# Performance work log

Measured on AMD Instinct MI355X. Metric: run time of the kernel, lower is better.

The kernel has to match this reference:

```python
import jax, jax.numpy as jnp
import numpy as np

N = 131072
IN, HID, OUT = 128, 256, 64
NUM_TASKS = 16
NUM_COPIES = 4
NUM_LAYERS = 3


def setup_inputs() -> dict:
    key = jax.random.key(0)
    ks = jax.random.split(key, 10)
    inputs = jax.random.normal(ks[0], (N, IN), dtype=jnp.float32)
    task_indices = jax.random.randint(ks[1], (N,), 0, NUM_TASKS, dtype=jnp.int32)
    copy_maps = jax.random.randint(ks[2], (NUM_LAYERS, NUM_TASKS), 0, NUM_COPIES, dtype=jnp.int32)
    # per-copy Linear weights, Kaiming-ish scale 1/sqrt(fan_in)
    W0 = jax.random.normal(ks[3], (NUM_COPIES, IN, HID), dtype=jnp.float32) / np.sqrt(IN)
    b0 = jax.random.normal(ks[4], (NUM_COPIES, HID), dtype=jnp.float32) * 0.01
    W1 = jax.random.normal(ks[5], (NUM_COPIES, HID, HID), dtype=jnp.float32) / np.sqrt(HID)
    b1 = jax.random.normal(ks[6], (NUM_COPIES, HID), dtype=jnp.float32) * 0.01
    W2 = jax.random.normal(ks[7], (NUM_COPIES, HID, OUT), dtype=jnp.float32) / np.sqrt(HID)
    b2 = jax.random.normal(ks[8], (NUM_COPIES, OUT), dtype=jnp.float32) * 0.01
    return {"inputs": inputs, "task_indices": task_indices, "copy_maps": copy_maps,
            "W0": W0, "b0": b0, "W1": W1, "b1": b1, "W2": W2, "b2": b2}


def _routed_layer(x, W, b, copy_idx, apply_tanh):
    # x: [N, d_in], W: [C, d_in, d_out], b: [C, d_out], copy_idx: [N]
    # Each token goes through exactly one copy's Linear. Equivalent to the
    # torch sort->per-copy-forward->unsort, expressed as masked accumulation
    # over the small fixed set of copies (avoids data-dependent shapes).
    y = jnp.zeros((x.shape[0], W.shape[2]), dtype=x.dtype)
    for c in range(W.shape[0]):
        mask = (copy_idx == c).astype(x.dtype)[:, None]  # [N, 1]
        y = y + mask * (x @ W[c] + b[c])
    return jnp.tanh(y) if apply_tanh else y


def reference(inputs, task_indices, copy_maps, W0, b0, W1, b1, W2, b2):
    x = inputs
    Ws = (W0, W1, W2)
    bs = (b0, b1, b2)
    for layer in range(NUM_LAYERS):
        copy_idx = copy_maps[layer][task_indices]  # [N] task->copy routing
        x = _routed_layer(x, Ws[layer], bs[layer], copy_idx,
                          apply_tanh=(layer != NUM_LAYERS - 1))
    return x
```

## Files before the change

kernel.cpp:

```cpp
#include <hip/hip_runtime.h>

#define N_TOK 131072
#define TILE 32
#define NT_MAX 4112

typedef __attribute__((ext_vector_type(8))) short s8v;
typedef __attribute__((ext_vector_type(4))) float f4v;
typedef unsigned short ushort_t;

__device__ __forceinline__ unsigned short f2bf(float x) {
    union { float f; unsigned u; } v; v.f = x;
    unsigned r = v.u + 0x7fffu + ((v.u >> 16) & 1u);
    return (unsigned short)(r >> 16);
}

__device__ __forceinline__ unsigned pk2(float a, float b) {
    union { float f; unsigned u; } x, y; x.f = a; y.f = b;
    return __byte_perm(x.u + 0x8000u, y.u + 0x8000u, 0x7632);
}

__device__ __forceinline__ float tanh_fast(float x) {
    float e = __expf(2.0f * x);
    float r = __builtin_amdgcn_rcpf(e + 1.0f);
    return __builtin_fmaf(-2.0f, r, 1.0f);
}

__global__ void prep_hist_kernel(const float* __restrict__ W0, const float* __restrict__ W1,
                                 const float* __restrict__ W2,
                                 ushort_t* __restrict__ W0p, ushort_t* __restrict__ W1p,
                                 ushort_t* __restrict__ W2p,
                                 const int* __restrict__ task, int* __restrict__ blockCounts) {
    if (blockIdx.x < 224) {
        int f = blockIdx.x * 256 + threadIdx.x;
        const float* src; ushort_t* dst; int K, N;
        if (f < 16384)      { src = W0; dst = W0p; K = 128; N = 256; }
        else if (f < 49152) { src = W1; dst = W1p; K = 256; N = 256; f -= 16384; }
        else                { src = W2; dst = W2p; K = 256; N = 64;  f -= 49152; }
        int fpc = (N >> 4) * (K >> 5) * 64;
        int c = f / fpc, r = f % fpc;
        int lane = r & 63;
        int kt = (r >> 6) % (K >> 5);
        int ftile = (r >> 6) / (K >> 5);
        int n = ftile * 16 + (lane & 15);
        int kbase = kt * 32 + (lane >> 4) * 8;
        const float* s = src + (size_t)c * K * N + (size_t)kbase * N + n;
        s8v pk;
#pragma unroll
        for (int j = 0; j < 8; j++) pk[j] = (short)f2bf(s[(size_t)j * N]);
        *reinterpret_cast<s8v*>(dst + ((size_t)(c * fpc + r) << 3)) = pk;
    } else {
        __shared__ int cnt[16];
        int t = threadIdx.x;
        int hb = blockIdx.x - 224;
        if (t < 16) cnt[t] = 0;
        __syncthreads();
        int base = hb * 2048 + t;
#pragma unroll
        for (int i = 0; i < 8; i++) atomicAdd(&cnt[task[base + i * 256]], 1);
        __syncthreads();
        if (t < 16) blockCounts[hb * 16 + t] = cnt[t];
    }
}

__global__ void sort_kernel(const int* __restrict__ task, const int* __restrict__ blockCounts,
                            int* __restrict__ tileTask, int* __restrict__ nT,
                            int* __restrict__ perm) {
    __shared__ int cntLds[1024];
    __shared__ int total[16], pref[16], rank[16];
    __shared__ int tokBase[16], tbase[17];
    int t = threadIdx.x, b = blockIdx.x;
    for (int i = t; i < 1024; i += 256) cntLds[i] = blockCounts[i];
    if (t < 16) rank[t] = 0;
    __syncthreads();
    if (t < 16) {
        int tot = 0, pf = 0;
#pragma unroll
        for (int bb = 0; bb < 64; bb++) {
            int v = cntLds[bb * 16 + t];
            tot += v;
            if (bb < b) pf += v;
        }
        total[t] = tot; pref[t] = pf;
    }
    __syncthreads();
    if (t == 0) {
        int tok = 0, tile = 0;
        for (int k = 0; k < 16; k++) {
            tokBase[k] = tok;
            tbase[k] = tile;
            int ntk = (total[k] + TILE - 1) / TILE;
            tok += ntk * TILE;
            tile += ntk;
        }
        tbase[16] = tile;
        if (b == 0) nT[0] = tile;
    }
    __syncthreads();
    if (b == 0) {
        for (int i = t; i < NT_MAX; i += 256) {
            int tk = 0;
            if (i < tbase[16]) {
#pragma unroll
                for (int k = 0; k < 16; k++) if (i >= tbase[k]) tk = k;
            }
            tileTask[i] = tk;
        }
    }
    int tk[8], my[8];
#pragma unroll
    for (int i = 0; i < 8; i++) {
        int idx = b * 2048 + i * 256 + t;
        tk[i] = task[idx];
        my[i] = atomicAdd(&rank[tk[i]], 1);
    }
#pragma unroll
    for (int i = 0; i < 8; i++) {
        int idx = b * 2048 + i * 256 + t;
        perm[tokBase[tk[i]] + pref[tk[i]] + my[i]] = idx;
    }
}

__launch_bounds__(512, 8)
__global__ void mlp_kernel(const float* __restrict__ x_in,
                           const int* __restrict__ cmap,
                           const float* __restrict__ b0,
                           const float* __restrict__ b1,
                           const float* __restrict__ b2,
                           const ushort_t* __restrict__ W0p,
                           const ushort_t* __restrict__ W1p,
                           const ushort_t* __restrict__ W2p,
                           const int* __restrict__ tileTask,
                           const int* __restrict__ nTp,
                           const int* __restrict__ perm,
                           float* __restrict__ out) {
    __shared__ __align__(16) ushort_t H1[8192];
    __shared__ __align__(16) ushort_t XH2[8192];
    __shared__ int toks[TILE];

    int b = blockIdx.x;
    if (b >= nTp[0]) return;
    int t = threadIdx.x;
    int task = tileTask[b];
    int c0 = cmap[task], c1 = cmap[16 + task], c2 = cmap[32 + task];

    int w = t >> 6;
    int lane = t & 63;
    int l15 = lane & 15, lq = lane >> 4;

    {
        int r = t >> 4, q = t & 15;
        int tok = perm[b * TILE + r];
        if (q == 0) toks[r] = tok;
        float4 v0 = make_float4(0.f, 0.f, 0.f, 0.f), v1 = v0;
        if ((unsigned)tok < (unsigned)N_TOK) {
            const float4* src = reinterpret_cast<const float4*>(x_in) + (size_t)tok * 32 + q * 2;
            v0 = src[0]; v1 = src[1];
        }
        int fragid = (r >> 4) * 4 + (q >> 2);
        int lanep = (r & 15) + 16 * (q & 3);
        uint4 pk;
        pk.x = pk2(v0.x, v0.y); pk.y = pk2(v0.z, v0.w);
        pk.z = pk2(v1.x, v1.y); pk.w = pk2(v1.z, v1.w);
        *reinterpret_cast<uint4*>(&XH2[(fragid * 64 + lanep) << 3]) = pk;
    }
    __syncthreads();

    {
        f4v acc[2][2];
#pragma unroll
        for (int mi = 0; mi < 2; mi++) {
            float4 bv = *reinterpret_cast<const float4*>(b0 + c0 * 256 + (2 * w + mi) * 16 + lq * 4);
#pragma unroll
            for (int nt = 0; nt < 2; nt++) {
                acc[mi][nt][0] = bv.x; acc[mi][nt][1] = bv.y;
                acc[mi][nt][2] = bv.z; acc[mi][nt][3] = bv.w;
            }
        }
        const ushort_t* Wc = W0p + (size_t)c0 * 32768;
#pragma unroll
        for (int kt = 0; kt < 4; kt++) {
            s8v wa[2];
#pragma unroll
            for (int mi = 0; mi < 2; mi++)
                wa[mi] = *reinterpret_cast<const s8v*>(Wc + ((((2 * w + mi) * 4 + kt) * 64 + lane) << 3));
            s8v xb[2];
#pragma unroll
            for (int nt = 0; nt < 2; nt++)
                xb[nt] = *reinterpret_cast<const s8v*>(&XH2[((nt * 4 + kt) * 64 + lane) << 3]);
#pragma unroll
            for (int mi = 0; mi < 2; mi++)
#pragma unroll
                for (int nt = 0; nt < 2; nt++)
                    acc[mi][nt] = __builtin_amdgcn_mfma_f32_16x16x32_bf16(wa[mi], xb[nt], acc[mi][nt], 0, 0, 0);
        }
#pragma unroll
        for (int mi = 0; mi < 2; mi++) {
            int ft = 2 * w + mi;
            int kt_h = ft >> 1;
            int lanep = l15 + 16 * ((ft & 1) * 2 + (lq >> 1));
            int j0 = (lq & 1) * 4;
#pragma unroll
            for (int nt = 0; nt < 2; nt++) {
                float t0 = tanh_fast(acc[mi][nt][0]);
                float t1 = tanh_fast(acc[mi][nt][1]);
                float t2 = tanh_fast(acc[mi][nt][2]);
                float t3 = tanh_fast(acc[mi][nt][3]);
                uint2 pk; pk.x = pk2(t0, t1); pk.y = pk2(t2, t3);
                *reinterpret_cast<uint2*>(&H1[(((nt * 8 + kt_h) * 64 + lanep) << 3) + j0]) = pk;
            }
        }
    }
    __syncthreads();

    {
        f4v acc[2][2];
#pragma unroll
        for (int mi = 0; mi < 2; mi++) {
            float4 bv = *reinterpret_cast<const float4*>(b1 + c1 * 256 + (2 * w + mi) * 16 + lq * 4);
#pragma unroll
            for (int nt = 0; nt < 2; nt++) {
                acc[mi][nt][0] = bv.x; acc[mi][nt][1] = bv.y;
                acc[mi][nt][2] = bv.z; acc[mi][nt][3] = bv.w;
            }
        }
        const ushort_t* Wc = W1p + (size_t)c1 * 65536;
#pragma unroll
        for (int kt = 0; kt < 8; kt++) {
            s8v wa[2];
#pragma unroll
            for (int mi = 0; mi < 2; mi++)
                wa[mi] = *reinterpret_cast<const s8v*>(Wc + ((((2 * w + mi) * 8 + kt) * 64 + lane) << 3));
            s8v xb[2];
#pragma unroll
            for (int nt = 0; nt < 2; nt++)
                xb[nt] = *reinterpret_cast<const s8v*>(&H1[((nt * 8 + kt) * 64 + lane) << 3]);
#pragma unroll
            for (int mi = 0; mi < 2; mi++)
#pragma unroll
                for (int nt = 0; nt < 2; nt++)
                    acc[mi][nt] = __builtin_amdgcn_mfma_f32_16x16x32_bf16(wa[mi], xb[nt], acc[mi][nt], 0, 0, 0);
        }
#pragma unroll
        for (int mi = 0; mi < 2; mi++) {
            int ft = 2 * w + mi;
            int kt_h = ft >> 1;
            int lanep = l15 + 16 * ((ft & 1) * 2 + (lq >> 1));
            int j0 = (lq & 1) * 4;
#pragma unroll
            for (int nt = 0; nt < 2; nt++) {
                float t0 = tanh_fast(acc[mi][nt][0]);
                float t1 = tanh_fast(acc[mi][nt][1]);
                float t2 = tanh_fast(acc[mi][nt][2]);
                float t3 = tanh_fast(acc[mi][nt][3]);
                uint2 pk; pk.x = pk2(t0, t1); pk.y = pk2(t2, t3);
                *reinterpret_cast<uint2*>(&XH2[(((nt * 8 + kt_h) * 64 + lanep) << 3) + j0]) = pk;
            }
        }
    }
    __syncthreads();

    {
        int mt = w & 3, nt = w >> 2;
        float4 bv = *reinterpret_cast<const float4*>(b2 + c2 * 64 + mt * 16 + lq * 4);
        f4v acc;
        acc[0] = bv.x; acc[1] = bv.y; acc[2] = bv.z; acc[3] = bv.w;
        const ushort_t* Wc = W2p + (size_t)c2 * 16384;
#pragma unroll
        for (int kt = 0; kt < 8; kt++) {
            s8v wa = *reinterpret_cast<const s8v*>(Wc + (((mt * 8 + kt) * 64 + lane) << 3));
            s8v xb = *reinterpret_cast<const s8v*>(&XH2[((nt * 8 + kt) * 64 + lane) << 3]);
            acc = __builtin_amdgcn_mfma_f32_16x16x32_bf16(wa, xb, acc, 0, 0, 0);
        }
        int tok = toks[nt * 16 + l15];
        if ((unsigned)tok < (unsigned)N_TOK) {
            float4 o;
            o.x = acc[0]; o.y = acc[1]; o.z = acc[2]; o.w = acc[3];
            *reinterpret_cast<float4*>(out + (size_t)tok * 64 + mt * 16 + lq * 4) = o;
        }
    }
}

extern "C" void kernel_launch(void* const* d_in, const int* in_sizes, int n_in,
                              void* d_out, int out_size, void* d_ws, size_t ws_size,
                              hipStream_t stream) {
    const float* inputs = (const float*)d_in[0];
    const int*   task   = (const int*)d_in[1];
    const int*   cmap   = (const int*)d_in[2];
    const float* W0     = (const float*)d_in[3];
    const float* b0     = (const float*)d_in[4];
    const float* W1     = (const float*)d_in[5];
    const float* b1     = (const float*)d_in[6];
    const float* W2     = (const float*)d_in[7];
    const float* b2     = (const float*)d_in[8];
    float* out = (float*)d_out;

    char* ws = (char*)d_ws;
    int* blockCounts = (int*)(ws + 0);
    int* nT          = (int*)(ws + 4096);
    int* tileTask    = (int*)(ws + 4160);
    int* perm        = (int*)(ws + 20608);
    ushort_t* W0p    = (ushort_t*)(ws + 546944);
    ushort_t* W1p    = (ushort_t*)(ws + 809088);
    ushort_t* W2p    = (ushort_t*)(ws + 1333376);

    prep_hist_kernel<<<288, 256, 0, stream>>>(W0, W1, W2, W0p, W1p, W2p, task, blockCounts);
    sort_kernel<<<64, 256, 0, stream>>>(task, blockCounts, tileTask, nT, perm);
    mlp_kernel<<<NT_MAX, 512, 0, stream>>>(inputs, cmap, b0, b1, b2,
                                           W0p, W1p, W2p, tileTask, nT, perm, out);
}
```

Before: 167.3 us.

## Double token tile to 64 per block to halve weight fetches per token

Raises the token tile from 32 to 64, so each block runs four N-fragments per wave and each weight fragment loaded from global memory feeds twice as many MFMAs. LDS buffers double, the launch-bounds occupancy hint drops from 8 to 4, and the grid is halved. Padding slots in perm are now set to -1 explicitly in the sort kernel, and the final layer reads token ids from perm instead of a shared array. The trade is fewer resident blocks and higher register use against less weight traffic and less per-block overhead.

```diff
diff --git a/kernel.cpp b/kernel.cpp
--- a/kernel.cpp
+++ b/kernel.cpp
@@ -1,8 +1,8 @@
 #include <hip/hip_runtime.h>
 
 #define N_TOK 131072
-#define TILE 32
-#define NT_MAX 4112
+#define TILE 64
+#define NT_MAX 2064
 
 typedef __attribute__((ext_vector_type(8))) short s8v;
 typedef __attribute__((ext_vector_type(4))) float f4v;
@@ -105,6 +105,12 @@
             }
             tileTask[i] = tk;
         }
+        for (int i = t; i < 16 * TILE; i += 256) {
+            int k = i >> 6, off = i & (TILE - 1);
+            int idx = total[k] + off;
+            int lim = ((total[k] + TILE - 1) / TILE) * TILE;
+            if (idx < lim) perm[tokBase[k] + idx] = -1;
+        }
     }
     int tk[8], my[8];
 #pragma unroll
@@ -120,7 +126,7 @@
     }
 }
 
-__launch_bounds__(512, 8)
+__launch_bounds__(512, 4)
 __global__ void mlp_kernel(const float* __restrict__ x_in,
                            const int* __restrict__ cmap,
                            const float* __restrict__ b0,
@@ -133,9 +139,8 @@
                            const int* __restrict__ nTp,
                            const int* __restrict__ perm,
                            float* __restrict__ out) {
-    __shared__ __align__(16) ushort_t H1[8192];
-    __shared__ __align__(16) ushort_t XH2[8192];
-    __shared__ int toks[TILE];
+    __shared__ __align__(16) ushort_t H1[16384];
+    __shared__ __align__(16) ushort_t XH2[16384];
 
     int b = blockIdx.x;
     if (b >= nTp[0]) return;
@@ -148,30 +153,32 @@
     int l15 = lane & 15, lq = lane >> 4;
 
     {
-        int r = t >> 4, q = t & 15;
+        int r = t >> 3, q = t & 7;
         int tok = perm[b * TILE + r];
-        if (q == 0) toks[r] = tok;
-        float4 v0 = make_float4(0.f, 0.f, 0.f, 0.f), v1 = v0;
+        float4 v0 = make_float4(0.f, 0.f, 0.f, 0.f), v1 = v0, v2 = v0, v3 = v0;
         if ((unsigned)tok < (unsigned)N_TOK) {
-            const float4* src = reinterpret_cast<const float4*>(x_in) + (size_t)tok * 32 + q * 2;
-            v0 = src[0]; v1 = src[1];
-        }
-        int fragid = (r >> 4) * 4 + (q >> 2);
-        int lanep = (r & 15) + 16 * (q & 3);
-        uint4 pk;
-        pk.x = pk2(v0.x, v0.y); pk.y = pk2(v0.z, v0.w);
-        pk.z = pk2(v1.x, v1.y); pk.w = pk2(v1.z, v1.w);
-        *reinterpret_cast<uint4*>(&XH2[(fragid * 64 + lanep) << 3]) = pk;
+            const float4* src = reinterpret_cast<const float4*>(x_in) + (size_t)tok * 32 + q * 4;
+            v0 = src[0]; v1 = src[1]; v2 = src[2]; v3 = src[3];
+        }
+        int fragid = (r >> 4) * 4 + (q >> 1);
+        int lp0 = (r & 15) + 16 * ((q & 1) * 2);
+        uint4 pk0, pk1;
+        pk0.x = pk2(v0.x, v0.y); pk0.y = pk2(v0.z, v0.w);
+        pk0.z = pk2(v1.x, v1.y); pk0.w = pk2(v1.z, v1.w);
+        pk1.x = pk2(v2.x, v2.y); pk1.y = pk2(v2.z, v2.w);
+        pk1.z = pk2(v3.x, v3.y); pk1.w = pk2(v3.z, v3.w);
+        *reinterpret_cast<uint4*>(&XH2[(fragid * 64 + lp0) << 3]) = pk0;
+        *reinterpret_cast<uint4*>(&XH2[(fragid * 64 + lp0 + 16) << 3]) = pk1;
     }
     __syncthreads();
 
     {
-        f4v acc[2][2];
+        f4v acc[2][4];
 #pragma unroll
         for (int mi = 0; mi < 2; mi++) {
             float4 bv = *reinterpret_cast<const float4*>(b0 + c0 * 256 + (2 * w + mi) * 16 + lq * 4);
 #pragma unroll
-            for (int nt = 0; nt < 2; nt++) {
+            for (int nt = 0; nt < 4; nt++) {
                 acc[mi][nt][0] = bv.x; acc[mi][nt][1] = bv.y;
                 acc[mi][nt][2] = bv.z; acc[mi][nt][3] = bv.w;
             }
@@ -183,14 +190,14 @@
 #pragma unroll
             for (int mi = 0; mi < 2; mi++)
                 wa[mi] = *reinterpret_cast<const s8v*>(Wc + ((((2 * w + mi) * 4 + kt) * 64 + lane) << 3));
-            s8v xb[2];
-#pragma unroll
-            for (int nt = 0; nt < 2; nt++)
+            s8v xb[4];
+#pragma unroll
+            for (int nt = 0; nt < 4; nt++)
                 xb[nt] = *reinterpret_cast<const s8v*>(&XH2[((nt * 4 + kt) * 64 + lane) << 3]);
 #pragma unroll
             for (int mi = 0; mi < 2; mi++)
 #pragma unroll
-                for (int nt = 0; nt < 2; nt++)
+                for (int nt = 0; nt < 4; nt++)
                     acc[mi][nt] = __builtin_amdgcn_mfma_f32_16x16x32_bf16(wa[mi], xb[nt], acc[mi][nt], 0, 0, 0);
         }
 #pragma unroll
@@ -200,7 +207,7 @@
             int lanep = l15 + 16 * ((ft & 1) * 2 + (lq >> 1));
             int j0 = (lq & 1) * 4;
 #pragma unroll
-            for (int nt = 0; nt < 2; nt++) {
+            for (int nt = 0; nt < 4; nt++) {
                 float t0 = tanh_fast(acc[mi][nt][0]);
                 float t1 = tanh_fast(acc[mi][nt][1]);
                 float t2 = tanh_fast(acc[mi][nt][2]);
@@ -213,12 +220,12 @@
     __syncthreads();
 
     {
-        f4v acc[2][2];
+        f4v acc[2][4];
 #pragma unroll
         for (int mi = 0; mi < 2; mi++) {
             float4 bv = *reinterpret_cast<const float4*>(b1 + c1 * 256 + (2 * w + mi) * 16 + lq * 4);
 #pragma unroll
-            for (int nt = 0; nt < 2; nt++) {
+            for (int nt = 0; nt < 4; nt++) {
                 acc[mi][nt][0] = bv.x; acc[mi][nt][1] = bv.y;
                 acc[mi][nt][2] = bv.z; acc[mi][nt][3] = bv.w;
             }
@@ -230,14 +237,14 @@
 #pragma unroll
             for (int mi = 0; mi < 2; mi++)
                 wa[mi] = *reinterpret_cast<const s8v*>(Wc + ((((2 * w + mi) * 8 + kt) * 64 + lane) << 3));
-            s8v xb[2];
-#pragma unroll
-            for (int nt = 0; nt < 2; nt++)
+            s8v xb[4];
+#pragma unroll
+            for (int nt = 0; nt < 4; nt++)
                 xb[nt] = *reinterpret_cast<const s8v*>(&H1[((nt * 8 + kt) * 64 + lane) << 3]);
 #pragma unroll
             for (int mi = 0; mi < 2; mi++)
 #pragma unroll
-                for (int nt = 0; nt < 2; nt++)
+                for (int nt = 0; nt < 4; nt++)
                     acc[mi][nt] = __builtin_amdgcn_mfma_f32_16x16x32_bf16(wa[mi], xb[nt], acc[mi][nt], 0, 0, 0);
         }
 #pragma unroll
@@ -247,7 +254,7 @@
             int lanep = l15 + 16 * ((ft & 1) * 2 + (lq >> 1));
             int j0 = (lq & 1) * 4;
 #pragma unroll
-            for (int nt = 0; nt < 2; nt++) {
+            for (int nt = 0; nt < 4; nt++) {
                 float t0 = tanh_fast(acc[mi][nt][0]);
                 float t1 = tanh_fast(acc[mi][nt][1]);
                 float t2 = tanh_fast(acc[mi][nt][2]);
@@ -260,22 +267,32 @@
     __syncthreads();
 
     {
-        int mt = w & 3, nt = w >> 2;
+        int mt = w & 3, ntb = (w >> 2) * 2;
         float4 bv = *reinterpret_cast<const float4*>(b2 + c2 * 64 + mt * 16 + lq * 4);
-        f4v acc;
-        acc[0] = bv.x; acc[1] = bv.y; acc[2] = bv.z; acc[3] = bv.w;
+        f4v acc[2];
+#pragma unroll
+        for (int e = 0; e < 2; e++) {
+            acc[e][0] = bv.x; acc[e][1] = bv.y; acc[e][2] = bv.z; acc[e][3] = bv.w;
+        }
         const ushort_t* Wc = W2p + (size_t)c2 * 16384;
 #pragma unroll
         for (int kt = 0; kt < 8; kt++) {
             s8v wa = *reinterpret_cast<const s8v*>(Wc + (((mt * 8 + kt) * 64 + lane) << 3));
-            s8v xb = *reinterpret_cast<const s8v*>(&XH2[((nt * 8 + kt) * 64 + lane) << 3]);
-            acc = __builtin_amdgcn_mfma_f32_16x16x32_bf16(wa, xb, acc, 0, 0, 0);
-        }
-        int tok = toks[nt * 16 + l15];
-        if ((unsigned)tok < (unsigned)N_TOK) {
-            float4 o;
-            o.x = acc[0]; o.y = acc[1]; o.z = acc[2]; o.w = acc[3];
-            *reinterpret_cast<float4*>(out + (size_t)tok * 64 + mt * 16 + lq * 4) = o;
+#pragma unroll
+            for (int e = 0; e < 2; e++) {
+                s8v xb = *reinterpret_cast<const s8v*>(&XH2[(((ntb + e) * 8 + kt) * 64 + lane) << 3]);
+                acc[e] = __builtin_amdgcn_mfma_f32_16x16x32_bf16(wa, xb, acc[e], 0, 0, 0);
+            }
+        }
+#pragma unroll
+        for (int e = 0; e < 2; e++) {
+            int nt = ntb + e;
+            int tok = perm[b * TILE + nt * 16 + l15];
+            if ((unsigned)tok < (unsigned)N_TOK) {
+                float4 o;
+                o.x = acc[e][0]; o.y = acc[e][1]; o.z = acc[e][2]; o.w = acc[e][3];
+                *reinterpret_cast<float4*>(out + (size_t)tok * 64 + mt * 16 + lq * 4) = o;
+            }
         }
     }
 }
@@ -298,10 +315,10 @@
     int* blockCounts = (int*)(ws + 0);
     int* nT          = (int*)(ws + 4096);
     int* tileTask    = (int*)(ws + 4160);
-    int* perm        = (int*)(ws + 20608);
-    ushort_t* W0p    = (ushort_t*)(ws + 546944);
-    ushort_t* W1p    = (ushort_t*)(ws + 809088);
-    ushort_t* W2p    = (ushort_t*)(ws + 1333376);
+    int* perm        = (int*)(ws + 12416);
+    ushort_t* W0p    = (ushort_t*)(ws + 540800);
+    ushort_t* W1p    = (ushort_t*)(ws + 802944);
+    ushort_t* W2p    = (ushort_t*)(ws + 1327232);
 
     prep_hist_kernel<<<288, 256, 0, stream>>>(W0, W1, W2, W0p, W1p, W2p, task, blockCounts);
     sort_kernel<<<64, 256, 0, stream>>>(task, blockCounts, tileTask, nT, perm);
```

After: 162.2 us. 1.03x faster.

## Halve MLP block size to 4 waves with doubled per-wave MFMA tiles

Applied to the files above, without the earlier changes.

Shrinks the fused MLP kernel from 512 to 256 threads per block, so each wave computes four M-fragments instead of two in layers 0 and 1, and both N-tiles in layer 2. This reuses each loaded B fragment across more MFMAs and drops the shared-memory token list by reading perm directly. It also adds s_setprio around MFMA bursts and swaps __expf for a direct exp2 intrinsic in tanh. The sort kernel now writes -1 into padding slots of perm so the padded rows are skipped safely. Per-wave register pressure rises and the thread count per CU may fall.

```diff
diff --git a/kernel.cpp b/kernel.cpp
--- a/kernel.cpp
+++ b/kernel.cpp
@@ -20,7 +20,7 @@
 }
 
 __device__ __forceinline__ float tanh_fast(float x) {
-    float e = __expf(2.0f * x);
+    float e = __builtin_amdgcn_exp2f(x * 2.8853900817779268f);
     float r = __builtin_amdgcn_rcpf(e + 1.0f);
     return __builtin_fmaf(-2.0f, r, 1.0f);
 }
@@ -105,6 +105,12 @@
             }
             tileTask[i] = tk;
         }
+        for (int i = t; i < 16 * TILE; i += 256) {
+            int k = i >> 5, off = i & (TILE - 1);
+            int idx = total[k] + off;
+            int lim = ((total[k] + TILE - 1) / TILE) * TILE;
+            if (idx < lim) perm[tokBase[k] + idx] = -1;
+        }
     }
     int tk[8], my[8];
 #pragma unroll
@@ -120,7 +126,7 @@
     }
 }
 
-__launch_bounds__(512, 8)
+__launch_bounds__(256, 4)
 __global__ void mlp_kernel(const float* __restrict__ x_in,
                            const int* __restrict__ cmap,
                            const float* __restrict__ b0,
@@ -135,7 +141,6 @@
                            float* __restrict__ out) {
     __shared__ __align__(16) ushort_t H1[8192];
     __shared__ __align__(16) ushort_t XH2[8192];
-    __shared__ int toks[TILE];
 
     int b = blockIdx.x;
     if (b >= nTp[0]) return;
@@ -148,54 +153,54 @@
     int l15 = lane & 15, lq = lane >> 4;
 
     {
-        int r = t >> 4, q = t & 15;
+        int r = t >> 3, q = t & 7;
         int tok = perm[b * TILE + r];
-        if (q == 0) toks[r] = tok;
-        float4 v0 = make_float4(0.f, 0.f, 0.f, 0.f), v1 = v0;
+        float4 v0 = make_float4(0.f, 0.f, 0.f, 0.f), v1 = v0, v2 = v0, v3 = v0;
         if ((unsigned)tok < (unsigned)N_TOK) {
-            const float4* src = reinterpret_cast<const float4*>(x_in) + (size_t)tok * 32 + q * 2;
-            v0 = src[0]; v1 = src[1];
-        }
-        int fragid = (r >> 4) * 4 + (q >> 2);
-        int lanep = (r & 15) + 16 * (q & 3);
-        uint4 pk;
-        pk.x = pk2(v0.x, v0.y); pk.y = pk2(v0.z, v0.w);
-        pk.z = pk2(v1.x, v1.y); pk.w = pk2(v1.z, v1.w);
-        *reinterpret_cast<uint4*>(&XH2[(fragid * 64 + lanep) << 3]) = pk;
+            const float4* src = reinterpret_cast<const float4*>(x_in) + (size_t)tok * 32 + q * 4;
+            v0 = src[0]; v1 = src[1]; v2 = src[2]; v3 = src[3];
+        }
+        int fragid = (r >> 4) * 4 + (q >> 1);
+        int lp0 = (r & 15) + 16 * ((q & 1) * 2);
+        uint4 pk0, pk1;
+        pk0.x = pk2(v0.x, v0.y); pk0.y = pk2(v0.z, v0.w);
+        pk0.z = pk2(v1.x, v1.y); pk0.w = pk2(v1.z, v1.w);
+        pk1.x = pk2(v2.x, v2.y); pk1.y = pk2(v2.z, v2.w);
+        pk1.z = pk2(v3.x, v3.y); pk1.w = pk2(v3.z, v3.w);
+        *reinterpret_cast<uint4*>(&XH2[(fragid * 64 + lp0) << 3]) = pk0;
+        *reinterpret_cast<uint4*>(&XH2[(fragid * 64 + lp0 + 16) << 3]) = pk1;
     }
     __syncthreads();
 
     {
-        f4v acc[2][2];
-#pragma unroll
-        for (int mi = 0; mi < 2; mi++) {
-            float4 bv = *reinterpret_cast<const float4*>(b0 + c0 * 256 + (2 * w + mi) * 16 + lq * 4);
-#pragma unroll
-            for (int nt = 0; nt < 2; nt++) {
-                acc[mi][nt][0] = bv.x; acc[mi][nt][1] = bv.y;
-                acc[mi][nt][2] = bv.z; acc[mi][nt][3] = bv.w;
-            }
+        f4v acc[4][2];
+#pragma unroll
+        for (int mi = 0; mi < 4; mi++) {
+            f4v bv = *reinterpret_cast<const f4v*>(b0 + c0 * 256 + (4 * w + mi) * 16 + lq * 4);
+            acc[mi][0] = bv; acc[mi][1] = bv;
         }
         const ushort_t* Wc = W0p + (size_t)c0 * 32768;
 #pragma unroll
         for (int kt = 0; kt < 4; kt++) {
-            s8v wa[2];
-#pragma unroll
-            for (int mi = 0; mi < 2; mi++)
-                wa[mi] = *reinterpret_cast<const s8v*>(Wc + ((((2 * w + mi) * 4 + kt) * 64 + lane) << 3));
+            s8v wa[4];
+#pragma unroll
+            for (int mi = 0; mi < 4; mi++)
+                wa[mi] = *reinterpret_cast<const s8v*>(Wc + ((((4 * w + mi) * 4 + kt) * 64 + lane) << 3));
             s8v xb[2];
 #pragma unroll
             for (int nt = 0; nt < 2; nt++)
                 xb[nt] = *reinterpret_cast<const s8v*>(&XH2[((nt * 4 + kt) * 64 + lane) << 3]);
-#pragma unroll
-            for (int mi = 0; mi < 2; mi++)
+            __builtin_amdgcn_s_setprio(1);
+#pragma unroll
+            for (int mi = 0; mi < 4; mi++)
 #pragma unroll
                 for (int nt = 0; nt < 2; nt++)
                     acc[mi][nt] = __builtin_amdgcn_mfma_f32_16x16x32_bf16(wa[mi], xb[nt], acc[mi][nt], 0, 0, 0);
-        }
-#pragma unroll
-        for (int mi = 0; mi < 2; mi++) {
-            int ft = 2 * w + mi;
+            __builtin_amdgcn_s_setprio(0);
+        }
+#pragma unroll
+        for (int mi = 0; mi < 4; mi++) {
+            int ft = 4 * w + mi;
             int kt_h = ft >> 1;
             int lanep = l15 + 16 * ((ft & 1) * 2 + (lq >> 1));
             int j0 = (lq & 1) * 4;
@@ -213,36 +218,34 @@
     __syncthreads();
 
     {
-        f4v acc[2][2];
-#pragma unroll
-        for (int mi = 0; mi < 2; mi++) {
-            float4 bv = *reinterpret_cast<const float4*>(b1 + c1 * 256 + (2 * w + mi) * 16 + lq * 4);
-#pragma unroll
-            for (int nt = 0; nt < 2; nt++) {
-                acc[mi][nt][0] = bv.x; acc[mi][nt][1] = bv.y;
-                acc[mi][nt][2] = bv.z; acc[mi][nt][3] = bv.w;
-            }
+        f4v acc[4][2];
+#pragma unroll
+        for (int mi = 0; mi < 4; mi++) {
+            f4v bv = *reinterpret_cast<const f4v*>(b1 + c1 * 256 + (4 * w + mi) * 16 + lq * 4);
+            acc[mi][0] = bv; acc[mi][1] = bv;
         }
         const ushort_t* Wc = W1p + (size_t)c1 * 65536;
 #pragma unroll
         for (int kt = 0; kt < 8; kt++) {
-            s8v wa[2];
-#pragma unroll
-            for (int mi = 0; mi < 2; mi++)
-                wa[mi] = *reinterpret_cast<const s8v*>(Wc + ((((2 * w + mi) * 8 + kt) * 64 + lane) << 3));
+            s8v wa[4];
+#pragma unroll
+            for (int mi = 0; mi < 4; mi++)
+                wa[mi] = *reinterpret_cast<const s8v*>(Wc + ((((4 * w + mi) * 8 + kt) * 64 + lane) << 3));
             s8v xb[2];
 #pragma unroll
             for (int nt = 0; nt < 2; nt++)
                 xb[nt] = *reinterpret_cast<const s8v*>(&H1[((nt * 8 + kt) * 64 + lane) << 3]);
-#pragma unroll
-            for (int mi = 0; mi < 2; mi++)
+            __builtin_amdgcn_s_setprio(1);
+#pragma unroll
+            for (int mi = 0; mi < 4; mi++)
 #pragma unroll
                 for (int nt = 0; nt < 2; nt++)
                     acc[mi][nt] = __builtin_amdgcn_mfma_f32_16x16x32_bf16(wa[mi], xb[nt], acc[mi][nt], 0, 0, 0);
-        }
-#pragma unroll
-        for (int mi = 0; mi < 2; mi++) {
-            int ft = 2 * w + mi;
+            __builtin_amdgcn_s_setprio(0);
+        }
+#pragma unroll
+        for (int mi = 0; mi < 4; mi++) {
+            int ft = 4 * w + mi;
             int kt_h = ft >> 1;
             int lanep = l15 + 16 * ((ft & 1) * 2 + (lq >> 1));
             int j0 = (lq & 1) * 4;
@@ -260,22 +263,30 @@
     __syncthreads();
 
     {
-        int mt = w & 3, nt = w >> 2;
-        float4 bv = *reinterpret_cast<const float4*>(b2 + c2 * 64 + mt * 16 + lq * 4);
-        f4v acc;
-        acc[0] = bv.x; acc[1] = bv.y; acc[2] = bv.z; acc[3] = bv.w;
+        int tok0 = perm[b * TILE + l15];
+        int tok1 = perm[b * TILE + 16 + l15];
+        f4v bv = *reinterpret_cast<const f4v*>(b2 + c2 * 64 + w * 16 + lq * 4);
+        f4v acc[2];
+        acc[0] = bv; acc[1] = bv;
         const ushort_t* Wc = W2p + (size_t)c2 * 16384;
 #pragma unroll
         for (int kt = 0; kt < 8; kt++) {
-            s8v wa = *reinterpret_cast<const s8v*>(Wc + (((mt * 8 + kt) * 64 + lane) << 3));
-            s8v xb = *reinterpret_cast<const s8v*>(&XH2[((nt * 8 + kt) * 64 + lane) << 3]);
-            acc = __builtin_amdgcn_mfma_f32_16x16x32_bf16(wa, xb, acc, 0, 0, 0);
-        }
-        int tok = toks[nt * 16 + l15];
-        if ((unsigned)tok < (unsigned)N_TOK) {
-            float4 o;
-            o.x = acc[0]; o.y = acc[1]; o.z = acc[2]; o.w = acc[3];
-            *reinterpret_cast<float4*>(out + (size_t)tok * 64 + mt * 16 + lq * 4) = o;
+            s8v wa = *reinterpret_cast<const s8v*>(Wc + (((w * 8 + kt) * 64 + lane) << 3));
+            s8v xb0 = *reinterpret_cast<const s8v*>(&XH2[((0 * 8 + kt) * 64 + lane) << 3]);
+            s8v xb1 = *reinterpret_cast<const s8v*>(&XH2[((1 * 8 + kt) * 64 + lane) << 3]);
+            __builtin_amdgcn_s_setprio(1);
+            acc[0] = __builtin_amdgcn_mfma_f32_16x16x32_bf16(wa, xb0, acc[0], 0, 0, 0);
+            acc[1] = __builtin_amdgcn_mfma_f32_16x16x32_bf16(wa, xb1, acc[1], 0, 0, 0);
+            __builtin_amdgcn_s_setprio(0);
+        }
+#pragma unroll
+        for (int e = 0; e < 2; e++) {
+            int tok = e ? tok1 : tok0;
+            if ((unsigned)tok < (unsigned)N_TOK) {
+                float4 o;
+                o.x = acc[e][0]; o.y = acc[e][1]; o.z = acc[e][2]; o.w = acc[e][3];
+                *reinterpret_cast<float4*>(out + (size_t)tok * 64 + w * 16 + lq * 4) = o;
+            }
         }
     }
 }
@@ -305,6 +316,6 @@
 
     prep_hist_kernel<<<288, 256, 0, stream>>>(W0, W1, W2, W0p, W1p, W2p, task, blockCounts);
     sort_kernel<<<64, 256, 0, stream>>>(task, blockCounts, tileTask, nT, perm);
-    mlp_kernel<<<NT_MAX, 512, 0, stream>>>(inputs, cmap, b0, b1, b2,
+    mlp_kernel<<<NT_MAX, 256, 0, stream>>>(inputs, cmap, b0, b1, b2,
                                            W0p, W1p, W2p, tileTask, nT, perm, out);
 }
```

Result: no change. 168.4 us (+0.7%).

## Prefetch next-layer weights into registers across layer barriers in fused MLP

Applied to the files above, without the earlier changes.

Weights for each layer are now loaded into registers during the previous layer's epilogue, and bias and token indices are loaded up front. LDS operand fragments are batched ahead of the MFMA chains, with sched_barrier calls to keep this ordering. Launch bounds are relaxed from 8 to 3 blocks per CU to give the prefetched fragments enough registers. Padding slots in perm are now explicitly set to -1, and tanh uses exp2 directly. The cost is more register pressure and possibly lower occupancy, traded for hiding global load latency behind compute.

```diff
diff --git a/kernel.cpp b/kernel.cpp
--- a/kernel.cpp
+++ b/kernel.cpp
@@ -20,7 +20,7 @@
 }
 
 __device__ __forceinline__ float tanh_fast(float x) {
-    float e = __expf(2.0f * x);
+    float e = __builtin_amdgcn_exp2f(x * 2.8853900817779268f);
     float r = __builtin_amdgcn_rcpf(e + 1.0f);
     return __builtin_fmaf(-2.0f, r, 1.0f);
 }
@@ -105,6 +105,12 @@
             }
             tileTask[i] = tk;
         }
+        for (int i = t; i < 16 * TILE; i += 256) {
+            int k = i >> 5, off = i & (TILE - 1);
+            int idx = total[k] + off;
+            int lim = ((total[k] + TILE - 1) / TILE) * TILE;
+            if (idx < lim) perm[tokBase[k] + idx] = -1;
+        }
     }
     int tk[8], my[8];
 #pragma unroll
@@ -120,7 +126,7 @@
     }
 }
 
-__launch_bounds__(512, 8)
+__launch_bounds__(512, 3)
 __global__ void mlp_kernel(const float* __restrict__ x_in,
                            const int* __restrict__ cmap,
                            const float* __restrict__ b0,
@@ -135,7 +141,6 @@
                            float* __restrict__ out) {
     __shared__ __align__(16) ushort_t H1[8192];
     __shared__ __align__(16) ushort_t XH2[8192];
-    __shared__ int toks[TILE];
 
     int b = blockIdx.x;
     if (b >= nTp[0]) return;
@@ -146,18 +151,38 @@
     int w = t >> 6;
     int lane = t & 63;
     int l15 = lane & 15, lq = lane >> 4;
+    int mt2 = w & 3, nt2 = w >> 2;
+
+    const ushort_t* Wc0 = W0p + (size_t)c0 * 32768;
+    const ushort_t* Wc1 = W1p + (size_t)c1 * 65536;
+    const ushort_t* Wc2 = W2p + (size_t)c2 * 16384;
+
+    int rS = t >> 4, qS = t & 15;
+    int tokS = perm[b * TILE + rS];
+    s8v wa0[2][4];
+#pragma unroll
+    for (int mi = 0; mi < 2; mi++)
+#pragma unroll
+        for (int kt = 0; kt < 4; kt++)
+            wa0[mi][kt] = *reinterpret_cast<const s8v*>(Wc0 + ((((2 * w + mi) * 4 + kt) * 64 + lane) << 3));
+    f4v bv0[2], bv1[2], bv2;
+#pragma unroll
+    for (int mi = 0; mi < 2; mi++) {
+        bv0[mi] = *reinterpret_cast<const f4v*>(b0 + c0 * 256 + (2 * w + mi) * 16 + lq * 4);
+        bv1[mi] = *reinterpret_cast<const f4v*>(b1 + c1 * 256 + (2 * w + mi) * 16 + lq * 4);
+    }
+    bv2 = *reinterpret_cast<const f4v*>(b2 + c2 * 64 + mt2 * 16 + lq * 4);
+    int tokO = perm[b * TILE + nt2 * 16 + l15];
+    __builtin_amdgcn_sched_barrier(0);
 
     {
-        int r = t >> 4, q = t & 15;
-        int tok = perm[b * TILE + r];
-        if (q == 0) toks[r] = tok;
         float4 v0 = make_float4(0.f, 0.f, 0.f, 0.f), v1 = v0;
-        if ((unsigned)tok < (unsigned)N_TOK) {
-            const float4* src = reinterpret_cast<const float4*>(x_in) + (size_t)tok * 32 + q * 2;
+        if ((unsigned)tokS < (unsigned)N_TOK) {
+            const float4* src = reinterpret_cast<const float4*>(x_in) + (size_t)tokS * 32 + qS * 2;
             v0 = src[0]; v1 = src[1];
         }
-        int fragid = (r >> 4) * 4 + (q >> 2);
-        int lanep = (r & 15) + 16 * (q & 3);
+        int fragid = (rS >> 4) * 4 + (qS >> 2);
+        int lanep = (rS & 15) + 16 * (qS & 3);
         uint4 pk;
         pk.x = pk2(v0.x, v0.y); pk.y = pk2(v0.z, v0.w);
         pk.z = pk2(v1.x, v1.y); pk.w = pk2(v1.z, v1.w);
@@ -165,34 +190,31 @@
     }
     __syncthreads();
 
+    s8v wa1a[2][4];
     {
+        s8v xb[2][4];
+#pragma unroll
+        for (int nt = 0; nt < 2; nt++)
+#pragma unroll
+            for (int kt = 0; kt < 4; kt++)
+                xb[nt][kt] = *reinterpret_cast<const s8v*>(&XH2[((nt * 4 + kt) * 64 + lane) << 3]);
+        __builtin_amdgcn_sched_barrier(0);
         f4v acc[2][2];
 #pragma unroll
-        for (int mi = 0; mi < 2; mi++) {
-            float4 bv = *reinterpret_cast<const float4*>(b0 + c0 * 256 + (2 * w + mi) * 16 + lq * 4);
-#pragma unroll
-            for (int nt = 0; nt < 2; nt++) {
-                acc[mi][nt][0] = bv.x; acc[mi][nt][1] = bv.y;
-                acc[mi][nt][2] = bv.z; acc[mi][nt][3] = bv.w;
-            }
-        }
-        const ushort_t* Wc = W0p + (size_t)c0 * 32768;
-#pragma unroll
-        for (int kt = 0; kt < 4; kt++) {
-            s8v wa[2];
+        for (int mi = 0; mi < 2; mi++) { acc[mi][0] = bv0[mi]; acc[mi][1] = bv0[mi]; }
+#pragma unroll
+        for (int kt = 0; kt < 4; kt++)
 #pragma unroll
             for (int mi = 0; mi < 2; mi++)
-                wa[mi] = *reinterpret_cast<const s8v*>(Wc + ((((2 * w + mi) * 4 + kt) * 64 + lane) << 3));
-            s8v xb[2];
-#pragma unroll
-            for (int nt = 0; nt < 2; nt++)
-                xb[nt] = *reinterpret_cast<const s8v*>(&XH2[((nt * 4 + kt) * 64 + lane) << 3]);
-#pragma unroll
-            for (int mi = 0; mi < 2; mi++)
 #pragma unroll
                 for (int nt = 0; nt < 2; nt++)
-                    acc[mi][nt] = __builtin_amdgcn_mfma_f32_16x16x32_bf16(wa[mi], xb[nt], acc[mi][nt], 0, 0, 0);
-        }
+                    acc[mi][nt] = __builtin_amdgcn_mfma_f32_16x16x32_bf16(wa0[mi][kt], xb[nt][kt], acc[mi][nt], 0, 0, 0);
+#pragma unroll
+        for (int mi = 0; mi < 2; mi++)
+#pragma unroll
+            for (int kt = 0; kt < 4; kt++)
+                wa1a[mi][kt] = *reinterpret_cast<const s8v*>(Wc1 + ((((2 * w + mi) * 8 + kt) * 64 + lane) << 3));
+        __builtin_amdgcn_sched_barrier(0);
 #pragma unroll
         for (int mi = 0; mi < 2; mi++) {
             int ft = 2 * w + mi;
@@ -212,34 +234,48 @@
     }
     __syncthreads();
 
+    s8v wa2[8];
     {
         f4v acc[2][2];
 #pragma unroll
-        for (int mi = 0; mi < 2; mi++) {
-            float4 bv = *reinterpret_cast<const float4*>(b1 + c1 * 256 + (2 * w + mi) * 16 + lq * 4);
-#pragma unroll
-            for (int nt = 0; nt < 2; nt++) {
-                acc[mi][nt][0] = bv.x; acc[mi][nt][1] = bv.y;
-                acc[mi][nt][2] = bv.z; acc[mi][nt][3] = bv.w;
-            }
-        }
-        const ushort_t* Wc = W1p + (size_t)c1 * 65536;
-#pragma unroll
-        for (int kt = 0; kt < 8; kt++) {
-            s8v wa[2];
+        for (int mi = 0; mi < 2; mi++) { acc[mi][0] = bv1[mi]; acc[mi][1] = bv1[mi]; }
+        s8v xba[2][4];
+#pragma unroll
+        for (int nt = 0; nt < 2; nt++)
+#pragma unroll
+            for (int kt = 0; kt < 4; kt++)
+                xba[nt][kt] = *reinterpret_cast<const s8v*>(&H1[((nt * 8 + kt) * 64 + lane) << 3]);
+        __builtin_amdgcn_sched_barrier(0);
+#pragma unroll
+        for (int kt = 0; kt < 4; kt++)
 #pragma unroll
             for (int mi = 0; mi < 2; mi++)
-                wa[mi] = *reinterpret_cast<const s8v*>(Wc + ((((2 * w + mi) * 8 + kt) * 64 + lane) << 3));
-            s8v xb[2];
-#pragma unroll
-            for (int nt = 0; nt < 2; nt++)
-                xb[nt] = *reinterpret_cast<const s8v*>(&H1[((nt * 8 + kt) * 64 + lane) << 3]);
+#pragma unroll
+                for (int nt = 0; nt < 2; nt++)
+                    acc[mi][nt] = __builtin_amdgcn_mfma_f32_16x16x32_bf16(wa1a[mi][kt], xba[nt][kt], acc[mi][nt], 0, 0, 0);
+        s8v wa1b[2][4], xbb[2][4];
+#pragma unroll
+        for (int mi = 0; mi < 2; mi++)
+#pragma unroll
+            for (int kt = 0; kt < 4; kt++)
+                wa1b[mi][kt] = *reinterpret_cast<const s8v*>(Wc1 + ((((2 * w + mi) * 8 + kt + 4) * 64 + lane) << 3));
+#pragma unroll
+        for (int nt = 0; nt < 2; nt++)
+#pragma unroll
+            for (int kt = 0; kt < 4; kt++)
+                xbb[nt][kt] = *reinterpret_cast<const s8v*>(&H1[((nt * 8 + kt + 4) * 64 + lane) << 3]);
+        __builtin_amdgcn_sched_barrier(0);
+#pragma unroll
+        for (int kt = 0; kt < 4; kt++)
 #pragma unroll
             for (int mi = 0; mi < 2; mi++)
 #pragma unroll
                 for (int nt = 0; nt < 2; nt++)
-                    acc[mi][nt] = __builtin_amdgcn_mfma_f32_16x16x32_bf16(wa[mi], xb[nt], acc[mi][nt], 0, 0, 0);
-        }
+                    acc[mi][nt] = __builtin_amdgcn_mfma_f32_16x16x32_bf16(wa1b[mi][kt], xbb[nt][kt], acc[mi][nt], 0, 0, 0);
+#pragma unroll
+        for (int kt = 0; kt < 8; kt++)
+            wa2[kt] = *reinterpret_cast<const s8v*>(Wc2 + (((mt2 * 8 + kt) * 64 + lane) << 3));
+        __builtin_amdgcn_sched_barrier(0);
 #pragma unroll
         for (int mi = 0; mi < 2; mi++) {
             int ft = 2 * w + mi;
@@ -260,22 +296,19 @@
     __syncthreads();
 
     {
-        int mt = w & 3, nt = w >> 2;
-        float4 bv = *reinterpret_cast<const float4*>(b2 + c2 * 64 + mt * 16 + lq * 4);
-        f4v acc;
-        acc[0] = bv.x; acc[1] = bv.y; acc[2] = bv.z; acc[3] = bv.w;
-        const ushort_t* Wc = W2p + (size_t)c2 * 16384;
-#pragma unroll
-        for (int kt = 0; kt < 8; kt++) {
-            s8v wa = *reinterpret_cast<const s8v*>(Wc + (((mt * 8 + kt) * 64 + lane) << 3));
-            s8v xb = *reinterpret_cast<const s8v*>(&XH2[((nt * 8 + kt) * 64 + lane) << 3]);
-            acc = __builtin_amdgcn_mfma_f32_16x16x32_bf16(wa, xb, acc, 0, 0, 0);
-        }
-        int tok = toks[nt * 16 + l15];
-        if ((unsigned)tok < (unsigned)N_TOK) {
+        s8v xb[8];
+#pragma unroll
+        for (int kt = 0; kt < 8; kt++)
+            xb[kt] = *reinterpret_cast<const s8v*>(&XH2[((nt2 * 8 + kt) * 64 + lane) << 3]);
+        __builtin_amdgcn_sched_barrier(0);
+        f4v acc = bv2;
+#pragma unroll
+        for (int kt = 0; kt < 8; kt++)
+            acc = __builtin_amdgcn_mfma_f32_16x16x32_bf16(wa2[kt], xb[kt], acc, 0, 0, 0);
+        if ((unsigned)tokO < (unsigned)N_TOK) {
             float4 o;
             o.x = acc[0]; o.y = acc[1]; o.z = acc[2]; o.w = acc[3];
-            *reinterpret_cast<float4*>(out + (size_t)tok * 64 + mt * 16 + lq * 4) = o;
+            *reinterpret_cast<float4*>(out + (size_t)tokO * 64 + mt2 * 16 + lq * 4) = o;
         }
     }
 }
```

Result: no change. 170.3 us (+1.8%).
